# Kernel optimization log

Hardware: AMD Instinct MI355X
Metric: run time of the kernel (lower is better)

Reference implementation:

```python
import jax, jax.numpy as jnp
import numpy as np

D_MODEL = 1024
NUM_HEADS = 16
EPS = 1e-5


def _layernorm(x, gamma, beta):
    mu = jnp.mean(x, axis=-1, keepdims=True)
    var = jnp.mean(jnp.square(x - mu), axis=-1, keepdims=True)
    return (x - mu) * jax.lax.rsqrt(var + EPS) * gamma + beta


def setup_inputs() -> dict:
    key = jax.random.key(0)
    ks = jax.random.split(key, 8)
    B, S, D = 4, 2048, D_MODEL
    xav = (6.0 / (D + D)) ** 0.5  # xavier_uniform bound for square D x D
    inp = {
        "q": jax.random.normal(ks[0], (B, S, D), dtype=jnp.float32),
        "k": jax.random.normal(ks[1], (B, S, D), dtype=jnp.float32),
        "v": jax.random.normal(ks[2], (B, S, D), dtype=jnp.float32),
        "Wq": jax.random.uniform(ks[3], (D, D), jnp.float32, -xav, xav),
        "Wk": jax.random.uniform(ks[4], (D, D), jnp.float32, -xav, xav),
        "Wv": jax.random.uniform(ks[5], (D, D), jnp.float32, -xav, xav),
        "Wo": jax.random.uniform(ks[6], (D, D), jnp.float32, -xav, xav),
        "bo": jnp.zeros((D,), jnp.float32),
        "q_gamma": jnp.ones((D,), jnp.float32),
        "q_beta": jnp.zeros((D,), jnp.float32),
        "k_gamma": jnp.ones((D,), jnp.float32),
        "k_beta": jnp.zeros((D,), jnp.float32),
    }
    return inp


def reference(q, k, v, Wq, Wk, Wv, Wo, bo, q_gamma, q_beta, k_gamma, k_beta):
    B, S, D = q.shape
    H = NUM_HEADS
    scale = 1.0 / (D ** 0.5)  # NOTE: 1/sqrt(d_model), as in the source
    qp = _layernorm(q @ Wq, q_gamma, q_beta)  # LN over full d_model, pre-split
    kp = _layernorm(k @ Wk, k_gamma, k_beta)
    vp = v @ Wv
    qh = qp.reshape(B, S, H, D // H)  # [B,S,H,hd]
    kh = kp.reshape(B, S, H, D // H)
    vh = vp.reshape(B, S, H, D // H)
    attn = jnp.einsum("bqhd,bkhd->bhqk", qh, kh) * scale
    attn = jax.nn.softmax(attn, axis=-1)
    x = jnp.einsum("bhqk,bkhd->bqhd", attn, vh).reshape(B, S, D)
    return x @ Wo + bo
```

## Files before the change

### kernel.cpp

```cpp
#include <hip/hip_runtime.h>
#include <hip/hip_bf16.h>

typedef unsigned short u16;
typedef __attribute__((ext_vector_type(8))) short bf16x8;
typedef __attribute__((ext_vector_type(4))) float f32x4;
typedef __attribute__((ext_vector_type(16))) float f32x16;
typedef __attribute__((ext_vector_type(4))) unsigned short u16x4;
typedef __attribute__((ext_vector_type(4))) unsigned int u32x4;
typedef __attribute__((ext_vector_type(2))) int i32x2;

__device__ __forceinline__ u16 f2b(float f) {
    __hip_bfloat16 h = __float2bfloat16(f);
    u16 r; __builtin_memcpy(&r, &h, 2); return r;
}
__device__ __forceinline__ float bf2f(u16 u) {
    return __uint_as_float(((unsigned)u) << 16);
}
__device__ __forceinline__ void gload16(const void* g, void* l) {
    __builtin_amdgcn_global_load_lds(
        (const __attribute__((address_space(1))) unsigned int*)g,
        (__attribute__((address_space(3))) unsigned int*)l, 16, 0, 0);
}
__device__ __forceinline__ float fexp2(float x) {
    return __builtin_amdgcn_exp2f(x);
}
__device__ __forceinline__ unsigned cvtpk(float lo, float hi) {
    unsigned d;
    asm("v_cvt_pk_bf16_f32 %0, %1, %2" : "=v"(d) : "v"(lo), "v"(hi));
    return d;
}
__device__ __forceinline__ bf16x8 mk_pa(float a0, float a1, float a2, float a3,
                                        float b0, float b1, float b2, float b3) {
    int A0 = (int)cvtpk(a0, a1), A1 = (int)cvtpk(a2, a3);
    int B0 = (int)cvtpk(b0, b1), B1 = (int)cvtpk(b2, b3);
    i32x2 r0 = __builtin_amdgcn_permlane32_swap(A0, B0, false, false);
    i32x2 r1 = __builtin_amdgcn_permlane32_swap(A1, B1, false, false);
    u32x4 fw = { (unsigned)r0[0], (unsigned)r1[0], (unsigned)r0[1], (unsigned)r1[1] };
    return __builtin_bit_cast(bf16x8, fw);
}

__global__ __launch_bounds__(256)
void wt_kernel(const float* __restrict__ Wq, const float* __restrict__ Wk,
               const float* __restrict__ Wv, const float* __restrict__ Wo,
               u16* __restrict__ Wt) {
    const float* W = blockIdx.z == 0 ? Wq : blockIdx.z == 1 ? Wk : blockIdx.z == 2 ? Wv : Wo;
    u16* Out = Wt + (size_t)blockIdx.z * (1024 * 1024);
    __shared__ float T[64][65];
    const int t = threadIdx.x;
    const int r0 = blockIdx.y * 64, c0 = blockIdx.x * 64;
#pragma unroll
    for (int e = 0; e < 4; ++e) {
        int row = e * 16 + (t >> 4), c4 = (t & 15) * 4;
        f32x4 v = *(const f32x4*)(W + (r0 + row) * 1024 + c0 + c4);
        T[row][c4] = v[0]; T[row][c4 + 1] = v[1]; T[row][c4 + 2] = v[2]; T[row][c4 + 3] = v[3];
    }
    __syncthreads();
#pragma unroll
    for (int e = 0; e < 4; ++e) {
        int orow = e * 16 + (t >> 4), oc4 = (t & 15) * 4;
        u16x4 pk = { f2b(T[oc4][orow]), f2b(T[oc4 + 1][orow]),
                     f2b(T[oc4 + 2][orow]), f2b(T[oc4 + 3][orow]) };
        *(u16x4*)(Out + (c0 + orow) * 1024 + r0 + oc4) = pk;
    }
}

template <int AF32, int BIAS>
__device__ __forceinline__ void gemm_body(const void* __restrict__ Av,
                                          const u16* __restrict__ Bt,
                                          u16* __restrict__ Cb, float* __restrict__ Cf,
                                          const float* __restrict__ bias,
                                          u16* As, u16* Bs, int bx, int by) {
    constexpr int K = 1024;
    const int tid = threadIdx.x;
    const int lane = tid & 63, w = tid >> 6;
    const int wr = w >> 1, wc = w & 1;
    const int c = lane & 15, g = lane >> 4;
    const int m0 = by * 128, n0 = bx * 128;
    const int sr = lane >> 3, sc = (lane & 7) * 8;
    const float* Af = (const float*)Av;
    const u16* Ab = (const u16*)Av;
    f32x4 acc[4][4] = {};
    for (int kt = 0; kt < 16; ++kt) {
        const int k0 = kt * 64;
        if (AF32) {
#pragma unroll
            for (int i = 0; i < 8; ++i) {
                int idx = i * 256 + tid;
                int row = idx >> 4, c4 = (idx & 15) * 4;
                f32x4 v = *(const f32x4*)(Af + (size_t)(m0 + row) * K + k0 + c4);
                u16x4 pk = { f2b(v[0]), f2b(v[1]), f2b(v[2]), f2b(v[3]) };
                *(u16x4*)&As[row * 64 + c4] = pk;
            }
        } else {
#pragma unroll
            for (int i = 0; i < 4; ++i) {
                int row = 32 * w + 8 * i;
                gload16(Ab + (size_t)(m0 + row + sr) * K + k0 + sc, &As[row * 64]);
            }
        }
#pragma unroll
        for (int i = 0; i < 4; ++i) {
            int row = 32 * w + 8 * i;
            gload16(Bt + (size_t)(n0 + row + sr) * K + k0 + sc, &Bs[row * 64]);
        }
        __syncthreads();
#pragma unroll
        for (int kk = 0; kk < 2; ++kk) {
            bf16x8 af[4], bfr[4];
#pragma unroll
            for (int m = 0; m < 4; ++m)
                af[m] = *(const bf16x8*)&As[(wr * 64 + m * 16 + c) * 64 + kk * 32 + 8 * g];
#pragma unroll
            for (int n = 0; n < 4; ++n)
                bfr[n] = *(const bf16x8*)&Bs[(wc * 64 + n * 16 + c) * 64 + kk * 32 + 8 * g];
#pragma unroll
            for (int m = 0; m < 4; ++m)
#pragma unroll
                for (int n = 0; n < 4; ++n)
                    acc[m][n] = __builtin_amdgcn_mfma_f32_16x16x32_bf16(af[m], bfr[n], acc[m][n], 0, 0, 0);
        }
        __syncthreads();
    }
#pragma unroll
    for (int n = 0; n < 4; ++n) {
        int col = n0 + wc * 64 + n * 16 + c;
        float bv = BIAS ? bias[col] : 0.0f;
#pragma unroll
        for (int m = 0; m < 4; ++m) {
            int row0 = m0 + wr * 64 + m * 16 + 4 * g;
#pragma unroll
            for (int r = 0; r < 4; ++r) {
                if (BIAS) Cf[(row0 + r) * 1024 + col] = acc[m][n][r] + bv;
                else      Cb[(row0 + r) * 1024 + col] = f2b(acc[m][n][r]);
            }
        }
    }
}

__global__ __launch_bounds__(256)
void gemm_kernel_f(const u16* __restrict__ Ab, const u16* __restrict__ Bt,
                   float* __restrict__ Cf, const float* __restrict__ bias) {
    __shared__ u16 As[128 * 64];
    __shared__ u16 Bs[128 * 64];
    const int B = blockIdx.x;
    const int bx = (B >> 3) & 7;
    const int by = (B & 7) + 8 * (B >> 6);
    gemm_body<0, 1>(Ab, Bt, nullptr, Cf, bias, As, Bs, bx, by);
}

__global__ __launch_bounds__(256)
void gemm3_kernel(const float* __restrict__ q, const float* __restrict__ k,
                  const float* __restrict__ v, const u16* __restrict__ Wt,
                  u16* __restrict__ C3) {
    constexpr int K = 1024;
    __shared__ u16 As[128 * 64];
    __shared__ u16 Bs[256 * 64];
    const int B = blockIdx.x;
    const int bx = (B >> 3) & 3;
    const int p = (B & 7) + 8 * (B >> 5);
    const int by = p & 63;
    const int z = p >> 6;
    const float* Af = z == 0 ? q : z == 1 ? k : v;
    const u16* Bt = Wt + (size_t)z * 1048576;
    u16* Cb = C3 + (size_t)z * 8388608;

    const int tid = threadIdx.x;
    const int lane = tid & 63, w = tid >> 6;
    const int wr = w >> 1, wc = w & 1;
    const int c = lane & 15, g = lane >> 4;
    const int m0 = by * 128, n0 = bx * 256;
    const int sr = lane >> 3, sc = (lane & 7) * 8;
    f32x4 acc[4][8] = {};
    for (int kt = 0; kt < 16; ++kt) {
        const int k0 = kt * 64;
#pragma unroll
        for (int i = 0; i < 8; ++i) {
            int idx = i * 256 + tid;
            int row = idx >> 4, c4 = (idx & 15) * 4;
            f32x4 vv = *(const f32x4*)(Af + (size_t)(m0 + row) * K + k0 + c4);
            u16x4 pk = { f2b(vv[0]), f2b(vv[1]), f2b(vv[2]), f2b(vv[3]) };
            *(u16x4*)&As[row * 64 + c4] = pk;
        }
#pragma unroll
        for (int i = 0; i < 8; ++i) {
            int m = w * 8 + i;
            gload16(Bt + (size_t)(n0 + 8 * m + sr) * K + k0 + sc, &Bs[8 * m * 64]);
        }
        __syncthreads();
#pragma unroll
        for (int kk = 0; kk < 2; ++kk) {
            bf16x8 af[4], bfr[8];
#pragma unroll
            for (int m = 0; m < 4; ++m)
                af[m] = *(const bf16x8*)&As[(wr * 64 + m * 16 + c) * 64 + kk * 32 + 8 * g];
#pragma unroll
            for (int n = 0; n < 8; ++n)
                bfr[n] = *(const bf16x8*)&Bs[(wc * 128 + n * 16 + c) * 64 + kk * 32 + 8 * g];
#pragma unroll
            for (int m = 0; m < 4; ++m)
#pragma unroll
                for (int n = 0; n < 8; ++n)
                    acc[m][n] = __builtin_amdgcn_mfma_f32_16x16x32_bf16(af[m], bfr[n], acc[m][n], 0, 0, 0);
        }
        __syncthreads();
    }
#pragma unroll
    for (int n = 0; n < 8; ++n) {
        int col = n0 + wc * 128 + n * 16 + c;
#pragma unroll
        for (int m = 0; m < 4; ++m) {
            int row0 = m0 + wr * 64 + m * 16 + 4 * g;
#pragma unroll
            for (int r = 0; r < 4; ++r)
                Cb[(row0 + r) * 1024 + col] = f2b(acc[m][n][r]);
        }
    }
}

__global__ __launch_bounds__(256)
void gemm1_kernel(const float* __restrict__ Af, const u16* __restrict__ Bt,
                  u16* __restrict__ Cb) {
    __shared__ u16 As[128 * 64];
    __shared__ u16 Bs[128 * 64];
    const int B = blockIdx.x;
    const int bx = (B >> 3) & 7;
    const int by = (B & 7) + 8 * (B >> 6);
    gemm_body<1, 0>((const void*)Af, Bt, Cb, nullptr, nullptr, As, Bs, bx, by);
}

__device__ __forceinline__ void ln_body(const u16* __restrict__ P,
                                        const float* __restrict__ gamma,
                                        const float* __restrict__ beta,
                                        float mul, u16* __restrict__ Out) {
    const int row = blockIdx.x;
    const int tid = threadIdx.x;
    const int lane = tid & 63, w = tid >> 6;
    u16x4 xr = *(const u16x4*)(P + row * 1024 + tid * 4);
    float x0 = bf2f(xr[0]), x1 = bf2f(xr[1]), x2 = bf2f(xr[2]), x3 = bf2f(xr[3]);
    float s = x0 + x1 + x2 + x3;
    float sq = x0 * x0 + x1 * x1 + x2 * x2 + x3 * x3;
#pragma unroll
    for (int m = 1; m < 64; m <<= 1) { s += __shfl_xor(s, m); sq += __shfl_xor(sq, m); }
    __shared__ float red[8];
    if (lane == 0) { red[w] = s; red[4 + w] = sq; }
    __syncthreads();
    float st = red[0] + red[1] + red[2] + red[3];
    float sqt = red[4] + red[5] + red[6] + red[7];
    float mu = st * (1.0f / 1024.0f);
    float var = sqt * (1.0f / 1024.0f) - mu * mu;
    float rs = rsqrtf(var + 1e-5f);
    f32x4 gm = *(const f32x4*)(gamma + tid * 4);
    f32x4 bt = *(const f32x4*)(beta + tid * 4);
    float xs[4] = {x0, x1, x2, x3};
    u16x4 pk;
#pragma unroll
    for (int j = 0; j < 4; ++j)
        pk[j] = f2b(((xs[j] - mu) * rs * gm[j] + bt[j]) * mul);
    const int b = row >> 11, sI = row & 2047;
    const int col = tid * 4, hh = col >> 6, d = col & 63;
    *(u16x4*)(Out + (((b * 16 + hh) * 2048 + sI) << 6) + d) = pk;
}

__global__ __launch_bounds__(256)
void ln_kernel(const u16* __restrict__ P, const float* __restrict__ gamma,
               const float* __restrict__ beta, float mul, u16* __restrict__ Out) {
    ln_body(P, gamma, beta, mul, Out);
}

__global__ __launch_bounds__(256)
void ln2_kernel(const u16* __restrict__ P3,
                const float* __restrict__ qg, const float* __restrict__ qb,
                const float* __restrict__ kg, const float* __restrict__ kb,
                u16* __restrict__ Qa, u16* __restrict__ Ka, float mulq) {
    const int z = blockIdx.z;
    ln_body(P3 + (size_t)z * 8388608, z == 0 ? qg : kg, z == 0 ? qb : kb,
            z == 0 ? mulq : 1.0f, z == 0 ? Qa : Ka);
}

__global__ __launch_bounds__(256)
void vt_kernel(const u16* __restrict__ P, u16* __restrict__ Vt) {
    __shared__ u16 T[64][72];
    const int t = threadIdx.x;
    const int bh = blockIdx.y, s0 = blockIdx.x * 64;
    const int b = bh >> 4, h = bh & 15;
#pragma unroll
    for (int e = 0; e < 4; ++e) {
        int row = e * 16 + (t >> 4), c4 = (t & 15) * 4;
        u16x4 v = *(const u16x4*)(P + (b * 2048 + s0 + row) * 1024 + h * 64 + c4);
        *(u16x4*)&T[row][c4] = v;
    }
    __syncthreads();
#pragma unroll
    for (int e = 0; e < 4; ++e) {
        int dd = e * 16 + (t >> 4), s4 = (t & 15) * 4;
        u16x4 pk = { T[s4][dd], T[s4 + 1][dd], T[s4 + 2][dd], T[s4 + 3][dd] };
        *(u16x4*)(Vt + ((size_t)bh * 64 + dd) * 2048 + s0 + s4) = pk;
    }
}

__global__ __launch_bounds__(256, 4)
void attn_kernel(const u16* __restrict__ Qa, const u16* __restrict__ Ka,
                 const u16* __restrict__ Vt, u16* __restrict__ Xa) {
    __shared__ u16 Ks[2][4096];
    __shared__ u16 Vs[2][4096];
    const int tid = threadIdx.x;
    const int lane = tid & 63, w = tid >> 6;
    const int col = lane & 31, h = lane >> 5;
    const int bid = blockIdx.x;
    const int bh = (bid & 7) * 8 + ((bid >> 3) & 7);
    const int q0 = (bid >> 6) * 128;
    const int b = bh >> 4, hd = bh & 15;
    const int qb = q0 + w * 32;
    const int sw = (col & 7) << 4;

    const u16* qptr = Qa + ((size_t)bh * 2048 + qb + col) * 64;
    bf16x8 qf[4];
#pragma unroll
    for (int s = 0; s < 4; ++s)
        qf[s] = *(const bf16x8*)(qptr + 16 * s + 8 * h);

    const int sr = lane >> 3;
    const int scg = ((lane & 7) ^ sr) * 8;
    const u16* kA = Ka + ((size_t)bh * 2048 + sr) * 64 + scg;
    const u16* vA = Vt + ((size_t)bh * 64 + sr) * 2048 + scg;

    f32x16 o0 = {}, o1 = {};
    float li = 0.f;

#pragma unroll
    for (int j = 0; j < 2; ++j) {
        const int m = 2 * w + j;
        gload16(kA + (size_t)(8 * m) * 64, &Ks[0][8 * m * 64]);
        gload16(vA + (size_t)(8 * m) * 2048, &Vs[0][8 * m * 64]);
    }
    __syncthreads();

    int cur = 0;
    for (int t = 0; t < 32; ++t) {
        const int tn = (t + 1) & 31;
#pragma unroll
        for (int j = 0; j < 2; ++j) {
            const int m = 2 * w + j;
            gload16(kA + (size_t)(tn * 64 + 8 * m) * 64, &Ks[cur ^ 1][8 * m * 64]);
            gload16(vA + (size_t)(8 * m) * 2048 + tn * 64, &Vs[cur ^ 1][8 * m * 64]);
        }

        const char* kbase = (const char*)&Ks[cur][0];
        f32x16 sacc0 = {}, sacc1 = {};
        __builtin_amdgcn_s_setprio(1);
#pragma unroll
        for (int s = 0; s < 4; ++s) {
            bf16x8 kf0 = *(const bf16x8*)(kbase + (col) * 128       + ((32 * s + 16 * h) ^ sw));
            bf16x8 kf1 = *(const bf16x8*)(kbase + (32 + col) * 128  + ((32 * s + 16 * h) ^ sw));
            sacc0 = __builtin_amdgcn_mfma_f32_32x32x16_bf16(kf0, qf[s], sacc0, 0, 0, 0);
            sacc1 = __builtin_amdgcn_mfma_f32_32x32x16_bf16(kf1, qf[s], sacc1, 0, 0, 0);
        }
        __builtin_amdgcn_s_setprio(0);

        f32x16 p0, p1;
#pragma unroll
        for (int r = 0; r < 16; ++r) { p0[r] = fexp2(sacc0[r]); }
#pragma unroll
        for (int r = 0; r < 16; ++r) { p1[r] = fexp2(sacc1[r]); }
#pragma unroll
        for (int r = 0; r < 16; ++r) { li += p0[r] + p1[r]; }

        bf16x8 pa0 = mk_pa(p0[0], p0[1], p0[2], p0[3], p0[4], p0[5], p0[6], p0[7]);
        bf16x8 pa1 = mk_pa(p0[8], p0[9], p0[10], p0[11], p0[12], p0[13], p0[14], p0[15]);
        bf16x8 pa2 = mk_pa(p1[0], p1[1], p1[2], p1[3], p1[4], p1[5], p1[6], p1[7]);
        bf16x8 pa3 = mk_pa(p1[8], p1[9], p1[10], p1[11], p1[12], p1[13], p1[14], p1[15]);

        const char* vb = (const char*)&Vs[cur][0];
        __builtin_amdgcn_s_setprio(1);
#pragma unroll
        for (int sg = 0; sg < 4; ++sg) {
            bf16x8 pf = sg == 0 ? pa0 : sg == 1 ? pa1 : sg == 2 ? pa2 : pa3;
            const int cb = (32 * sg + 16 * h) ^ sw;
            bf16x8 vf0 = *(const bf16x8*)(vb + (col) * 128      + cb);
            bf16x8 vf1 = *(const bf16x8*)(vb + (32 + col) * 128 + cb);
            o0 = __builtin_amdgcn_mfma_f32_32x32x16_bf16(pf, vf0, o0, 0, 0, 0);
            o1 = __builtin_amdgcn_mfma_f32_32x32x16_bf16(pf, vf1, o1, 0, 0, 0);
        }
        __builtin_amdgcn_s_setprio(0);

        __syncthreads();
        cur ^= 1;
    }

    li += __shfl_xor(li, 32);
    float inv = 1.0f / li;
#pragma unroll
    for (int reg = 0; reg < 16; ++reg) {
        const int crow = (reg & 3) + 8 * (reg >> 2) + 4 * h;
        float ivr = __shfl(inv, crow);
        const int row = qb + crow;
        u16* xp = Xa + ((size_t)b * 2048 + row) * 1024 + hd * 64;
        xp[col] = f2b(o0[reg] * ivr);
        xp[32 + col] = f2b(o1[reg] * ivr);
    }
}

extern "C" void kernel_launch(void* const* d_in, const int* in_sizes, int n_in,
                              void* d_out, int out_size, void* d_ws, size_t ws_size,
                              hipStream_t stream) {
    const float* q   = (const float*)d_in[0];
    const float* k   = (const float*)d_in[1];
    const float* v   = (const float*)d_in[2];
    const float* Wq  = (const float*)d_in[3];
    const float* Wk  = (const float*)d_in[4];
    const float* Wv  = (const float*)d_in[5];
    const float* Wo  = (const float*)d_in[6];
    const float* bo  = (const float*)d_in[7];
    const float* qg  = (const float*)d_in[8];
    const float* qbt = (const float*)d_in[9];
    const float* kg  = (const float*)d_in[10];
    const float* kbt = (const float*)d_in[11];

    char* ws = (char*)d_ws;
    const float MUL_Q = 0.04508422002778f;

    if (ws_size >= 109051904ULL) {
        u16* Wt  = (u16*)(ws);
        u16* Qa  = (u16*)(ws + 8388608);
        u16* Ka  = (u16*)(ws + 25165824);
        u16* Vt  = (u16*)(ws + 41943040);
        u16* Pb3 = (u16*)(ws + 58720256);
        u16* Xa  = Pb3;

        wt_kernel<<<dim3(16, 16, 4), 256, 0, stream>>>(Wq, Wk, Wv, Wo, Wt);
        gemm3_kernel<<<768, 256, 0, stream>>>(q, k, v, Wt, Pb3);
        ln2_kernel<<<dim3(8192, 1, 2), 256, 0, stream>>>(Pb3, qg, qbt, kg, kbt, Qa, Ka, MUL_Q);
        vt_kernel<<<dim3(32, 64), 256, 0, stream>>>(Pb3 + 2 * 8388608, Vt);
        attn_kernel<<<1024, 256, 0, stream>>>(Qa, Ka, Vt, Xa);
        gemm_kernel_f<<<512, 256, 0, stream>>>((const u16*)Xa, Wt + 3145728, (float*)d_out, bo);
    } else {
        u16* Wt = (u16*)(ws);
        u16* Pb = (u16*)(ws + 8388608);
        u16* Qa = (u16*)(ws + 25165824);
        u16* Ka = (u16*)(ws + 41943040);
        u16* Vt = (u16*)(ws + 58720256);
        u16* Xa = Pb;

        wt_kernel<<<dim3(16, 16, 4), 256, 0, stream>>>(Wq, Wk, Wv, Wo, Wt);
        gemm1_kernel<<<512, 256, 0, stream>>>(q, Wt, Pb);
        ln_kernel<<<8192, 256, 0, stream>>>(Pb, qg, qbt, MUL_Q, Qa);
        gemm1_kernel<<<512, 256, 0, stream>>>(k, Wt + 1048576, Pb);
        ln_kernel<<<8192, 256, 0, stream>>>(Pb, kg, kbt, 1.0f, Ka);
        gemm1_kernel<<<512, 256, 0, stream>>>(v, Wt + 2097152, Pb);
        vt_kernel<<<dim3(32, 64), 256, 0, stream>>>(Pb, Vt);
        attn_kernel<<<1024, 256, 0, stream>>>(Qa, Ka, Vt, Xa);
        gemm_kernel_f<<<512, 256, 0, stream>>>((const u16*)Xa, Wt + 3145728, (float*)d_out, bo);
    }
}
```

Measured before the change: 265.5 us.

## Load fp32 A tiles directly to LDS and convert at fragment read in QKV GEMM

The fused QKV projection GEMM now streams fp32 activations straight into LDS with global_load_lds, using an XOR swizzle to avoid bank conflicts. The fp32 to bf16 conversion moves to fragment read time with packed cvt instructions. The tile shrinks from 128x256 to 128x128, doubling the grid to 1536 blocks. This removes the register round trip and scalar conversions in the A load path and gives more blocks for occupancy, at the cost of more LDS reads per MFMA and redundant B loads across the narrower tiles.

```diff
diff --git a/kernel.cpp b/kernel.cpp
--- a/kernel.cpp
+++ b/kernel.cpp
@@ -36,6 +36,11 @@
     i32x2 r0 = __builtin_amdgcn_permlane32_swap(A0, B0, false, false);
     i32x2 r1 = __builtin_amdgcn_permlane32_swap(A1, B1, false, false);
     u32x4 fw = { (unsigned)r0[0], (unsigned)r1[0], (unsigned)r0[1], (unsigned)r1[1] };
+    return __builtin_bit_cast(bf16x8, fw);
+}
+__device__ __forceinline__ bf16x8 pk8(f32x4 lo, f32x4 hi) {
+    u32x4 fw = { cvtpk(lo[0], lo[1]), cvtpk(lo[2], lo[3]),
+                 cvtpk(hi[0], hi[1]), cvtpk(hi[2], hi[3]) };
     return __builtin_bit_cast(bf16x8, fw);
 }
 
@@ -153,11 +158,11 @@
                   const float* __restrict__ v, const u16* __restrict__ Wt,
                   u16* __restrict__ C3) {
     constexpr int K = 1024;
-    __shared__ u16 As[128 * 64];
-    __shared__ u16 Bs[256 * 64];
+    __shared__ float Asf[128 * 64];
+    __shared__ u16 Bs[128 * 64];
     const int B = blockIdx.x;
-    const int bx = (B >> 3) & 3;
-    const int p = (B & 7) + 8 * (B >> 5);
+    const int bx = (B >> 3) & 7;
+    const int p = (B & 7) + 8 * (B >> 6);
     const int by = p & 63;
     const int z = p >> 6;
     const float* Af = z == 0 ? q : z == 1 ? k : v;
@@ -168,45 +173,53 @@
     const int lane = tid & 63, w = tid >> 6;
     const int wr = w >> 1, wc = w & 1;
     const int c = lane & 15, g = lane >> 4;
-    const int m0 = by * 128, n0 = bx * 256;
-    const int sr = lane >> 3, sc = (lane & 7) * 8;
-    f32x4 acc[4][8] = {};
+    const int m0 = by * 128, n0 = bx * 128;
+    const int arr = lane >> 4;
+    const int agr = (lane & 15) ^ arr;
+    const float* aS = Af + (size_t)(m0 + arr) * K + agr * 4;
+    const int srB = lane >> 3, scB = (lane & 7) * 8;
+    const u16* bS = Bt + (size_t)(n0 + srB) * K + scB;
+
+    const int s4r = c & 3;
+    f32x4 acc[4][4] = {};
     for (int kt = 0; kt < 16; ++kt) {
         const int k0 = kt * 64;
 #pragma unroll
         for (int i = 0; i < 8; ++i) {
-            int idx = i * 256 + tid;
-            int row = idx >> 4, c4 = (idx & 15) * 4;
-            f32x4 vv = *(const f32x4*)(Af + (size_t)(m0 + row) * K + k0 + c4);
-            u16x4 pk = { f2b(vv[0]), f2b(vv[1]), f2b(vv[2]), f2b(vv[3]) };
-            *(u16x4*)&As[row * 64 + c4] = pk;
-        }
-#pragma unroll
-        for (int i = 0; i < 8; ++i) {
             int m = w * 8 + i;
-            gload16(Bt + (size_t)(n0 + 8 * m + sr) * K + k0 + sc, &Bs[8 * m * 64]);
+            gload16(aS + (size_t)(4 * m) * K + k0, &Asf[4 * m * 64]);
+        }
+#pragma unroll
+        for (int i = 0; i < 4; ++i) {
+            int row = 32 * w + 8 * i;
+            gload16(bS + (size_t)row * K + k0, &Bs[row * 64]);
         }
         __syncthreads();
 #pragma unroll
         for (int kk = 0; kk < 2; ++kk) {
-            bf16x8 af[4], bfr[8];
+            bf16x8 af[4], bfr[4];
+#pragma unroll
+            for (int m = 0; m < 4; ++m) {
+                const int row = wr * 64 + m * 16 + c;
+                const int L0 = 8 * kk + 2 * g;
+                f32x4 lo = *(const f32x4*)&Asf[row * 64 + ((L0 ^ s4r) * 4)];
+                f32x4 hi = *(const f32x4*)&Asf[row * 64 + (((L0 + 1) ^ s4r) * 4)];
+                af[m] = pk8(lo, hi);
+            }
+#pragma unroll
+            for (int n = 0; n < 4; ++n)
+                bfr[n] = *(const bf16x8*)&Bs[(wc * 64 + n * 16 + c) * 64 + kk * 32 + 8 * g];
 #pragma unroll
             for (int m = 0; m < 4; ++m)
-                af[m] = *(const bf16x8*)&As[(wr * 64 + m * 16 + c) * 64 + kk * 32 + 8 * g];
-#pragma unroll
-            for (int n = 0; n < 8; ++n)
-                bfr[n] = *(const bf16x8*)&Bs[(wc * 128 + n * 16 + c) * 64 + kk * 32 + 8 * g];
-#pragma unroll
-            for (int m = 0; m < 4; ++m)
-#pragma unroll
-                for (int n = 0; n < 8; ++n)
+#pragma unroll
+                for (int n = 0; n < 4; ++n)
                     acc[m][n] = __builtin_amdgcn_mfma_f32_16x16x32_bf16(af[m], bfr[n], acc[m][n], 0, 0, 0);
         }
         __syncthreads();
     }
 #pragma unroll
-    for (int n = 0; n < 8; ++n) {
-        int col = n0 + wc * 128 + n * 16 + c;
+    for (int n = 0; n < 4; ++n) {
+        int col = n0 + wc * 64 + n * 16 + c;
 #pragma unroll
         for (int m = 0; m < 4; ++m) {
             int row0 = m0 + wr * 64 + m * 16 + 4 * g;
@@ -428,7 +441,7 @@
         u16* Xa  = Pb3;
 
         wt_kernel<<<dim3(16, 16, 4), 256, 0, stream>>>(Wq, Wk, Wv, Wo, Wt);
-        gemm3_kernel<<<768, 256, 0, stream>>>(q, k, v, Wt, Pb3);
+        gemm3_kernel<<<1536, 256, 0, stream>>>(q, k, v, Wt, Pb3);
         ln2_kernel<<<dim3(8192, 1, 2), 256, 0, stream>>>(Pb3, qg, qbt, kg, kbt, Qa, Ka, MUL_Q);
         vt_kernel<<<dim3(32, 64), 256, 0, stream>>>(Pb3 + 2 * 8388608, Vt);
         attn_kernel<<<1024, 256, 0, stream>>>(Qa, Ka, Vt, Xa);
```

Result: faster. 251.4 us (-5.3%).
